# Kernel optimization log

Hardware: AMD Instinct MI355X
Metric: run time of the kernel (lower is better)

## Reference

```python
import jax, jax.numpy as jnp
import numpy as np

B, Z, H, T = 256, 512, 2048, 16
EPS = 1e-5

def _normalize(v):
    return v / (jnp.linalg.norm(v) + 1e-12)

def setup_inputs() -> dict:
    key = jax.random.key(0)
    ks = jax.random.split(key, 10)
    s = lambda fan: 1.0 / np.sqrt(fan)
    return {
        "z": jax.random.normal(ks[0], (B, Z), dtype=jnp.float32),
        "fc_w": jax.random.normal(ks[1], (Z, Z), dtype=jnp.float32) * s(Z),
        "fc_b": jnp.zeros((Z,), dtype=jnp.float32),
        "fc_u": _normalize(jax.random.normal(ks[2], (Z,), dtype=jnp.float32)),
        "w_ih": jax.random.normal(ks[3], (3 * H, Z), dtype=jnp.float32) * s(Z),
        "w_hh": jax.random.normal(ks[4], (3 * H, H), dtype=jnp.float32) * s(H),
        "b_ih": jnp.zeros((3 * H,), dtype=jnp.float32).at[H:2 * H].set(1.0),  # forget-gate bias init
        "b_hh": jnp.zeros((3 * H,), dtype=jnp.float32),
        "lin_w": jax.random.normal(ks[5], (Z, H), dtype=jnp.float32) * s(H),
        "lin_b": jnp.zeros((Z,), dtype=jnp.float32),
    }

def _spectral_norm(w, u):
    # one torch-style power iteration (u, v treated as constants)
    v = jax.lax.stop_gradient(_normalize(w.T @ u))
    u1 = jax.lax.stop_gradient(_normalize(w @ v))
    sigma = u1 @ (w @ v)
    return w / sigma

def reference(z, fc_w, fc_b, fc_u, w_ih, w_hh, b_ih, b_hh, lin_w, lin_b):
    # spectral-norm linear: h0 = z @ (W/sigma)^T + b
    w_sn = _spectral_norm(fc_w, fc_u)
    x0 = z @ w_sn.T + fc_b                      # [B, Z]
    h0 = jnp.zeros((B, H), dtype=z.dtype)       # initHidden

    def step(carry, _):
        x, h = carry
        gi = x @ w_ih.T + b_ih                  # [B, 3H]
        gh = h @ w_hh.T + b_hh                  # [B, 3H]
        i_r, i_z, i_n = jnp.split(gi, 3, axis=1)
        h_r, h_z, h_n = jnp.split(gh, 3, axis=1)
        r = jax.nn.sigmoid(i_r + h_r)
        u = jax.nn.sigmoid(i_z + h_z)
        n = jnp.tanh(i_n + r * h_n)
        h_new = (1.0 - u) * n + u * h
        x_new = h_new @ lin_w.T + lin_b         # [B, Z] fed back as next input
        return (x_new, h_new), x_new

    _, outs = jax.lax.scan(step, (x0, h0), None, length=T)  # [T, B, Z]

    # per-timestep BatchNorm1d(affine=False), training-mode batch stats
    mean = jnp.mean(outs, axis=1, keepdims=True)
    var = jnp.mean((outs - mean) ** 2, axis=1, keepdims=True)
    y = (outs - mean) / jnp.sqrt(var + EPS)     # [T, B, Z]

    y = jnp.transpose(y, (1, 0, 2))             # [B, T, Z]
    return y.reshape(-1, Z)                     # [B*T, Z]
```

## Files before the change

### kernel.cpp

```cpp
#include <hip/hip_runtime.h>
#include <hip/hip_bf16.h>
#include <cstdint>
#include <cstddef>

#define B_  256
#define Z_  512
#define H_  2048
#define T_  16
#define H3_ 6144

using short8  = __attribute__((ext_vector_type(8))) short;
using bf16x8  = __attribute__((ext_vector_type(8))) __bf16;
using f32x4   = __attribute__((ext_vector_type(4))) float;
using f32x16  = __attribute__((ext_vector_type(16))) float;

__device__ __forceinline__ f32x4 mfma_bf16(short8 a, short8 b, f32x4 c) {
  return __builtin_amdgcn_mfma_f32_16x16x32_bf16(
      __builtin_bit_cast(bf16x8, a), __builtin_bit_cast(bf16x8, b), c, 0, 0, 0);
}
__device__ __forceinline__ f32x16 mfma_bf16_32(short8 a, short8 b, f32x16 c) {
  return __builtin_amdgcn_mfma_f32_32x32x16_bf16(
      __builtin_bit_cast(bf16x8, a), __builtin_bit_cast(bf16x8, b), c, 0, 0, 0);
}

__device__ __forceinline__ unsigned short f2bf(float f) {
  unsigned int u = __builtin_bit_cast(unsigned int, f);
  u = (u + 0x7FFFu + ((u >> 16) & 1u)) >> 16;
  return (unsigned short)u;
}

__device__ __forceinline__ float sigmoidf_(float x) { return 1.0f / (1.0f + __expf(-x)); }

__device__ __forceinline__ int swz(int row, int chunk) {
  return row * 64 + ((chunk ^ (row & 7)) << 3);
}

__global__ __launch_bounds__(256, 2) void gru_step3(
    const unsigned short* __restrict__ A, int K,
    const unsigned short* __restrict__ Wr,
    const unsigned short* __restrict__ Wz,
    const unsigned short* __restrict__ Wn,
    const unsigned short* __restrict__ Whn,
    const float* __restrict__ cr, const float* __restrict__ cz,
    const float* __restrict__ cn, const float* __restrict__ chn,
    float hn_scale,
    const float* __restrict__ h_old,
    float* __restrict__ h_new,
    unsigned short* __restrict__ h_hist)
{
  __shared__ __align__(16) unsigned short sbuf[2][10240];
  __shared__ float LDSf[4][32][33];
  const int bid = blockIdx.x, tid = threadIdx.x;
  const int xcd = bid & 7, rst = bid >> 3;
  const int m_idx = rst & 7, gg = rst >> 3;
  const int grp = gg * 8 + xcd;
  const int m0 = m_idx * 32;
  const int gh0 = grp * 32;
  const int wave = tid >> 6, lane = tid & 63;
  const int lh = lane >> 5, l31 = lane & 31;

  const int arow = tid >> 3, achk = tid & 7;
  const int wrow = tid >> 1, wc0 = (tid & 1) * 4;
  const unsigned short* wsrc =
      (wrow < 32) ? Wr : (wrow < 64) ? Wz : (wrow < 96) ? Wn : Whn;
  const size_t aoff = (size_t)(m0 + arow) * K + achk * 8;
  const size_t woff = (size_t)(gh0 + (wrow & 31)) * K + wc0 * 8;
  const int sa_d = swz(arow, achk);
  const int sw_d0 = 2048 + swz(wrow, wc0 + 0);
  const int sw_d1 = 2048 + swz(wrow, wc0 + 1);
  const int sw_d2 = 2048 + swz(wrow, wc0 + 2);
  const int sw_d3 = 2048 + swz(wrow, wc0 + 3);

  uint4 Aa, Aw0, Aw1, Aw2, Aw3;
  uint4 Ba, Bw0, Bw1, Bw2, Bw3;

#define LDSET(a, w0, w1, w2, w3, k0)                      \
  {                                                        \
    const int kk_ = (k0);                                  \
    a  = *(const uint4*)(A    + aoff + kk_);               \
    w0 = *(const uint4*)(wsrc + woff + kk_);               \
    w1 = *(const uint4*)(wsrc + woff + kk_ + 8);           \
    w2 = *(const uint4*)(wsrc + woff + kk_ + 16);          \
    w3 = *(const uint4*)(wsrc + woff + kk_ + 24);          \
  }
#define STAGE(s, a, w0, w1, w2, w3)                        \
  {                                                        \
    unsigned short* b_ = sbuf[s];                          \
    *(uint4*)(b_ + sa_d)  = a;                             \
    *(uint4*)(b_ + sw_d0) = w0;                            \
    *(uint4*)(b_ + sw_d1) = w1;                            \
    *(uint4*)(b_ + sw_d2) = w2;                            \
    *(uint4*)(b_ + sw_d3) = w3;                            \
  }

  f32x16 acc = {};
#define COMP(s)                                                            \
  {                                                                        \
    const unsigned short* b_ = sbuf[s];                                    \
    _Pragma("unroll")                                                      \
    for (int ks = 0; ks < 4; ++ks) {                                       \
      short8 af = *(const short8*)(b_ + swz(l31, ks * 2 + lh));            \
      short8 wf = *(const short8*)(b_ + 2048 + swz(wave * 32 + l31, ks * 2 + lh)); \
      acc = mfma_bf16_32(af, wf, acc);                                     \
    }                                                                      \
  }

  const int nIter = K >> 6;
  LDSET(Aa, Aw0, Aw1, Aw2, Aw3, 0);
  LDSET(Ba, Bw0, Bw1, Bw2, Bw3, 64);
  for (int it = 0; it < nIter; it += 2) {
    STAGE(0, Aa, Aw0, Aw1, Aw2, Aw3);
    __syncthreads();
    { const int kn = (it + 2 < nIter) ? ((it + 2) << 6) : 0;
      LDSET(Aa, Aw0, Aw1, Aw2, Aw3, kn); }
    COMP(0);
    STAGE(1, Ba, Bw0, Bw1, Bw2, Bw3);
    __syncthreads();
    { const int kn = (it + 3 < nIter) ? ((it + 3) << 6) : 64;
      LDSET(Ba, Bw0, Bw1, Bw2, Bw3, kn); }
    COMP(1);
  }
#undef LDSET
#undef STAGE
#undef COMP

#pragma unroll
  for (int reg = 0; reg < 16; ++reg) {
    const int row = (reg & 3) + 8 * (reg >> 2) + 4 * lh;
    LDSf[wave][row][l31] = acc[reg];
  }
  __syncthreads();
  {
    const int row = tid >> 3, c0 = (tid & 7) * 4;
    const int grow = m0 + row;
#pragma unroll
    for (int j = 0; j < 4; ++j) {
      const int col = c0 + j;
      const int gcol = gh0 + col;
      const float R   = sigmoidf_(LDSf[0][row][col] + cr[gcol]);
      const float U   = sigmoidf_(LDSf[1][row][col] + cz[gcol]);
      const float HNv = hn_scale * LDSf[3][row][col] + chn[gcol];
      const float Nv  = tanhf(LDSf[2][row][col] + cn[gcol] + R * HNv);
      const float ho  = h_old ? h_old[(size_t)grow * H_ + gcol] : 0.0f;
      const float hv  = (1.0f - U) * Nv + U * ho;
      h_new[(size_t)grow * H_ + gcol]  = hv;
      h_hist[(size_t)grow * H_ + gcol] = f2bf(hv);
    }
  }
}

__global__ __launch_bounds__(256) void gemm_bt(
    const unsigned short* __restrict__ A,
    const unsigned short* __restrict__ Bw,
    int K,
    const float* __restrict__ addsrc, int add_ld,
    const float* __restrict__ bias,
    const float* __restrict__ scale_ptr,
    unsigned short* __restrict__ out_bf,
    float* __restrict__ out_f, int ldo)
{
  __shared__ unsigned short sA[32 * 64];
  __shared__ unsigned short sB[64 * 64];
  const int tid  = threadIdx.x;
  const int m0   = blockIdx.x * 32, n0 = blockIdx.y * 64;
  const int wave = tid >> 6, lane = tid & 63;
  const int wr = wave & 1, wc = wave >> 1;
  const int q = lane >> 4, c16 = lane & 15;
  const int lr = tid >> 3, lc8 = tid & 7;
  f32x4 acc0 = {}, acc1 = {};
  const size_t rowA  = (size_t)(m0 + lr) * K;
  const size_t rowB0 = (size_t)(n0 + lr) * K;
  const size_t rowB1 = (size_t)(n0 + 32 + lr) * K;
  for (int k0 = 0; k0 < K; k0 += 64) {
    const int gc = k0 + lc8 * 8;
    uint4 ra  = *(const uint4*)(A  + rowA  + gc);
    uint4 rb0 = *(const uint4*)(Bw + rowB0 + gc);
    uint4 rb1 = *(const uint4*)(Bw + rowB1 + gc);
    __syncthreads();
    *(uint4*)(sA + swz(lr, lc8))      = ra;
    *(uint4*)(sB + swz(lr, lc8))      = rb0;
    *(uint4*)(sB + swz(32 + lr, lc8)) = rb1;
    __syncthreads();
#pragma unroll
    for (int kk = 0; kk < 2; ++kk) {
      const int arow = wr * 16 + c16;
      short8 af = *(const short8*)(sA + swz(arow, kk * 4 + q));
      const int brow = wc * 32 + c16;
      short8 b0 = *(const short8*)(sB + swz(brow, kk * 4 + q));
      acc0 = mfma_bf16(af, b0, acc0);
      short8 b1 = *(const short8*)(sB + swz(brow + 16, kk * 4 + q));
      acc1 = mfma_bf16(af, b1, acc1);
    }
  }
  const float scale = scale_ptr ? *scale_ptr : 1.0f;
#pragma unroll
  for (int cf = 0; cf < 2; ++cf) {
    f32x4 a = cf ? acc1 : acc0;
#pragma unroll
    for (int v = 0; v < 4; ++v) {
      const int row = m0 + wr * 16 + q * 4 + v;
      const int col = n0 + wc * 32 + cf * 16 + c16;
      float val = a[v] * scale;
      if (addsrc) val += addsrc[(size_t)row * add_ld + col];
      if (bias)   val += bias[col];
      if (out_f)  out_f[(size_t)row * ldo + col] = val;
      if (out_bf) out_bf[(size_t)row * ldo + col] = f2bf(val);
    }
  }
}

__global__ __launch_bounds__(256) void gemm_bt64(
    const unsigned short* __restrict__ A,
    const unsigned short* __restrict__ Bw,
    int K,
    const float* __restrict__ addsrc, int add_ld,
    const float* __restrict__ bias,
    unsigned short* __restrict__ out_bf,
    float* __restrict__ out_f, int ldo)
{
  __shared__ unsigned short sA[64 * 64];
  __shared__ unsigned short sB[64 * 64];
  const int tid  = threadIdx.x;
  const int m0   = blockIdx.x * 64, n0 = blockIdx.y * 64;
  const int wave = tid >> 6, lane = tid & 63;
  const int wr = wave & 1, wc = wave >> 1;
  const int q = lane >> 4, c16 = lane & 15;
  const int lr = tid >> 3, lc8 = tid & 7;
  f32x4 acc[2][2] = {};
  const size_t aoff = (size_t)(m0 + lr) * K;
  const size_t boff = (size_t)(n0 + lr) * K;
  const size_t s32  = (size_t)32 * K;

  uint4 ra0, ra1, rb0, rb1;
  auto LOAD = [&](int k0) {
    const int gc = k0 + lc8 * 8;
    ra0 = *(const uint4*)(A  + aoff + gc);
    ra1 = *(const uint4*)(A  + aoff + s32 + gc);
    rb0 = *(const uint4*)(Bw + boff + gc);
    rb1 = *(const uint4*)(Bw + boff + s32 + gc);
  };

  const int nIter = K >> 6;
  LOAD(0);
  for (int it = 0; it < nIter; ++it) {
    __syncthreads();
    *(uint4*)(sA + swz(lr, lc8))      = ra0;
    *(uint4*)(sA + swz(lr + 32, lc8)) = ra1;
    *(uint4*)(sB + swz(lr, lc8))      = rb0;
    *(uint4*)(sB + swz(lr + 32, lc8)) = rb1;
    __syncthreads();
    if (it + 1 < nIter) LOAD((it + 1) << 6);
#pragma unroll
    for (int kk = 0; kk < 2; ++kk) {
      short8 af0 = *(const short8*)(sA + swz(wr * 32 + c16,      kk * 4 + q));
      short8 af1 = *(const short8*)(sA + swz(wr * 32 + 16 + c16, kk * 4 + q));
      short8 bf0 = *(const short8*)(sB + swz(wc * 32 + c16,      kk * 4 + q));
      short8 bf1 = *(const short8*)(sB + swz(wc * 32 + 16 + c16, kk * 4 + q));
      acc[0][0] = mfma_bf16(af0, bf0, acc[0][0]);
      acc[0][1] = mfma_bf16(af0, bf1, acc[0][1]);
      acc[1][0] = mfma_bf16(af1, bf0, acc[1][0]);
      acc[1][1] = mfma_bf16(af1, bf1, acc[1][1]);
    }
  }
#pragma unroll
  for (int i = 0; i < 2; ++i) {
#pragma unroll
    for (int j = 0; j < 2; ++j) {
#pragma unroll
      for (int v = 0; v < 4; ++v) {
        const int row = m0 + wr * 32 + i * 16 + q * 4 + v;
        const int col = n0 + wc * 32 + j * 16 + c16;
        float val = acc[i][j][v];
        if (addsrc) val += addsrc[(size_t)row * add_ld + col];
        if (bias)   val += bias[col];
        if (out_f)  out_f[(size_t)row * ldo + col] = val;
        if (out_bf) out_bf[(size_t)row * ldo + col] = f2bf(val);
      }
    }
  }
}

__global__ __launch_bounds__(256) void quant_all(
    const float* __restrict__ z, const float* __restrict__ fc_w,
    const float* __restrict__ w_ih, const float* __restrict__ w_hh,
    const float* __restrict__ lin_w,
    unsigned short* __restrict__ z_q, unsigned short* __restrict__ fc_w_q,
    unsigned short* __restrict__ w_ih_q, unsigned short* __restrict__ w_hhn_q,
    unsigned short* __restrict__ lin_w_q)
{
  const int i = blockIdx.x * 256 + threadIdx.x;
  if (i >= 2195456) return;
  const float4* src; ushort4* dst; int idx;
  if (i < 32768)        { src = (const float4*)z;     dst = (ushort4*)z_q;     idx = i; }
  else if (i < 98304)   { src = (const float4*)fc_w;  dst = (ushort4*)fc_w_q;  idx = i - 32768; }
  else if (i < 884736)  { src = (const float4*)w_ih;  dst = (ushort4*)w_ih_q;  idx = i - 98304; }
  else if (i < 1933312) { src = (const float4*)(w_hh + (size_t)2 * H_ * H_);
                          dst = (ushort4*)w_hhn_q;    idx = i - 884736; }
  else                  { src = (const float4*)lin_w; dst = (ushort4*)lin_w_q; idx = i - 1933312; }
  float4 v = src[idx];
  ushort4 o; o.x = f2bf(v.x); o.y = f2bf(v.y); o.z = f2bf(v.z); o.w = f2bf(v.w);
  dst[idx] = o;
}

__global__ __launch_bounds__(256) void transq(const float* __restrict__ s,
                                              unsigned short* __restrict__ d) {
  __shared__ float tile[32][33];
  const int tx = threadIdx.x & 31, ty = threadIdx.x >> 5;
  const int k0 = blockIdx.x * 32, z0 = blockIdx.y * 32;
#pragma unroll
  for (int j = 0; j < 4; ++j)
    tile[ty + j * 8][tx] = s[(size_t)(z0 + ty + j * 8) * H_ + k0 + tx];
  __syncthreads();
#pragma unroll
  for (int j = 0; j < 4; ++j)
    d[(size_t)(k0 + ty + j * 8) * Z_ + z0 + tx] = f2bf(tile[tx][ty + j * 8]);
}

__global__ void sigma1(const float* __restrict__ W, const float* __restrict__ u,
                       float* __restrict__ t1) {
  __shared__ float part[4][64];
  const int lane = threadIdx.x & 63, wv = threadIdx.x >> 6;
  const int col = blockIdx.x * 64 + lane;
  float s = 0.f;
  for (int r = wv * 128; r < wv * 128 + 128; ++r)
    s += W[(size_t)r * Z_ + col] * u[r];
  part[wv][lane] = s;
  __syncthreads();
  if (wv == 0)
    t1[col] = part[0][lane] + part[1][lane] + part[2][lane] + part[3][lane];
}

__global__ void sigma1b(const float* __restrict__ t1, float* __restrict__ invn) {
  __shared__ float red[256];
  int t = threadIdx.x;
  float v0 = t1[t], v1 = t1[t + 256];
  red[t] = v0 * v0 + v1 * v1;
  __syncthreads();
  for (int s = 128; s > 0; s >>= 1) {
    if (t < s) red[t] += red[t + s];
    __syncthreads();
  }
  if (t == 0) invn[0] = 1.0f / (sqrtf(red[0]) + 1e-12f);
}

__global__ void sigma2(const float* __restrict__ W, const float* __restrict__ t1,
                       const float* __restrict__ invn, float* __restrict__ t2) {
  const int lane = threadIdx.x & 63, wv = threadIdx.x >> 6;
  const int row = blockIdx.x * 4 + wv;
  float s = 0.f;
  for (int c = lane; c < Z_; c += 64) s += W[(size_t)row * Z_ + c] * t1[c];
#pragma unroll
  for (int off = 32; off > 0; off >>= 1) s += __shfl_down(s, off);
  if (lane == 0) t2[row] = s * invn[0];
}

__global__ void sigma3(const float* __restrict__ t2, float* __restrict__ inv_sig) {
  __shared__ float red[256];
  int t = threadIdx.x;
  float v0 = t2[t], v1 = t2[t + 256];
  red[t] = v0 * v0 + v1 * v1;
  __syncthreads();
  for (int s = 128; s > 0; s >>= 1) {
    if (t < s) red[t] += red[t + s];
    __syncthreads();
  }
  if (t == 0) {
    float s2  = red[0];
    float sig = s2 / (sqrtf(s2) + 1e-12f);
    inv_sig[0] = 1.0f / sig;
  }
}

__global__ __launch_bounds__(256) void dots_k(const float* __restrict__ w,
                                              const float* __restrict__ lb,
                                              float* __restrict__ dvec) {
  const int wave = threadIdx.x >> 6, lane = threadIdx.x & 63;
#pragma unroll
  for (int i = 0; i < 4; ++i) {
    int row = blockIdx.x * 16 + wave * 4 + i;
    float s = 0.f;
    for (int c = lane; c < Z_; c += 64) s += w[(size_t)row * Z_ + c] * lb[c];
#pragma unroll
    for (int off = 32; off > 0; off >>= 1) s += __shfl_down(s, off);
    if (lane == 0) dvec[row] = s;
  }
}

__global__ void consts_k(const float* __restrict__ b_ih, const float* __restrict__ b_hh,
                         const float* __restrict__ dvec,
                         float* __restrict__ c0r, float* __restrict__ c0z,
                         float* __restrict__ c0n,
                         float* __restrict__ c1r, float* __restrict__ c1z,
                         float* __restrict__ c1n, float* __restrict__ chn) {
  int j = blockIdx.x * 256 + threadIdx.x;
  float br = b_ih[j], bz = b_ih[H_ + j], bn = b_ih[2 * H_ + j];
  float hr = b_hh[j], hz = b_hh[H_ + j], hn = b_hh[2 * H_ + j];
  c0r[j] = br + hr; c0z[j] = bz + hz; c0n[j] = bn; chn[j] = hn;
  c1r[j] = br + hr + dvec[j];
  c1z[j] = bz + hz + dvec[H_ + j];
  c1n[j] = bn + dvec[2 * H_ + j];
}

__global__ __launch_bounds__(256) void bn_k(const float* __restrict__ outs,
                                            float* __restrict__ y) {
  __shared__ float s_sum[4][64], s_sq[4][64], s_mean[64], s_inv[64];
  const int t = blockIdx.x, zb = blockIdx.y;
  const int zl = threadIdx.x & 63, bp = threadIdx.x >> 6;
  const int z = zb * 64 + zl;
  float sum = 0.f, sq = 0.f;
  for (int b = bp * 64; b < bp * 64 + 64; ++b) {
    float v = outs[(size_t)(t * 256 + b) * Z_ + z];
    sum += v; sq += v * v;
  }
  s_sum[bp][zl] = sum; s_sq[bp][zl] = sq;
  __syncthreads();
  if (bp == 0) {
    float S = s_sum[0][zl] + s_sum[1][zl] + s_sum[2][zl] + s_sum[3][zl];
    float Q = s_sq[0][zl] + s_sq[1][zl] + s_sq[2][zl] + s_sq[3][zl];
    float mean = S * (1.0f / 256.0f);
    float var  = Q * (1.0f / 256.0f) - mean * mean;
    s_mean[zl] = mean;
    s_inv[zl]  = rsqrtf(var + 1e-5f);
  }
  __syncthreads();
  const float mean = s_mean[zl], inv = s_inv[zl];
  for (int b = bp * 64; b < bp * 64 + 64; ++b) {
    float v = outs[(size_t)(t * 256 + b) * Z_ + z];
    y[(size_t)(b * T_ + t) * Z_ + z] = (v - mean) * inv;
  }
}

extern "C" void kernel_launch(void* const* d_in, const int* in_sizes, int n_in,
                              void* d_out, int out_size, void* d_ws, size_t ws_size,
                              hipStream_t stream) {
  const float* z     = (const float*)d_in[0];
  const float* fc_w  = (const float*)d_in[1];
  const float* fc_b  = (const float*)d_in[2];
  const float* fc_u  = (const float*)d_in[3];
  const float* w_ih  = (const float*)d_in[4];
  const float* w_hh  = (const float*)d_in[5];
  const float* b_ih  = (const float*)d_in[6];
  const float* b_hh  = (const float*)d_in[7];
  const float* lin_w = (const float*)d_in[8];
  const float* lin_b = (const float*)d_in[9];
  float* out = (float*)d_out;

  char* ws = (char*)d_ws;
  size_t off = 0;
  auto alloc = [&](size_t bytes) -> void* {
    off = (off + 255) & ~(size_t)255;
    void* p = ws + off;
    off += bytes;
    return p;
  };
  unsigned short* w_ih_q   = (unsigned short*)alloc((size_t)H3_ * Z_ * 2);
  unsigned short* w_hhn_q  = (unsigned short*)alloc((size_t)H_ * H_ * 2);
  unsigned short* lin_w_q  = (unsigned short*)alloc((size_t)Z_ * H_ * 2);
  unsigned short* lin_wT_q = (unsigned short*)alloc((size_t)Z_ * H_ * 2);
  unsigned short* fc_w_q   = (unsigned short*)alloc((size_t)Z_ * Z_ * 2);
  unsigned short* z_q      = (unsigned short*)alloc((size_t)B_ * Z_ * 2);
  unsigned short* x0_q     = (unsigned short*)alloc((size_t)B_ * Z_ * 2);
  unsigned short* Wsum_r   = (unsigned short*)alloc((size_t)H_ * H_ * 2);
  unsigned short* Wsum_z   = (unsigned short*)alloc((size_t)H_ * H_ * 2);
  unsigned short* Wn_c     = (unsigned short*)alloc((size_t)H_ * H_ * 2);
  unsigned short* Hhist    = (unsigned short*)alloc((size_t)T_ * B_ * H_ * 2);
  float* h_f32 = (float*)alloc((size_t)2 * B_ * H_ * 4);
  float* outs  = (float*)alloc((size_t)T_ * B_ * Z_ * 4);
  float* c0r = (float*)alloc(H_ * 4);
  float* c0z = (float*)alloc(H_ * 4);
  float* c0n = (float*)alloc(H_ * 4);
  float* c1r = (float*)alloc(H_ * 4);
  float* c1z = (float*)alloc(H_ * 4);
  float* c1n = (float*)alloc(H_ * 4);
  float* chn = (float*)alloc(H_ * 4);
  float* dvec = (float*)alloc(H3_ * 4);
  float* t1v = (float*)alloc(Z_ * 4);
  float* t2v = (float*)alloc(Z_ * 4);
  float* invn = (float*)alloc(256);
  float* invsig = (float*)alloc(256);
  (void)in_sizes; (void)n_in; (void)out_size; (void)ws_size;

  quant_all<<<dim3((2195456 + 255) / 256), 256, 0, stream>>>(
      z, fc_w, w_ih, w_hh, lin_w, z_q, fc_w_q, w_ih_q, w_hhn_q, lin_w_q);
  transq<<<dim3(64, 16), 256, 0, stream>>>(lin_w, lin_wT_q);
  sigma1<<<8, 256, 0, stream>>>(fc_w, fc_u, t1v);
  sigma1b<<<1, 256, 0, stream>>>(t1v, invn);
  sigma2<<<128, 256, 0, stream>>>(fc_w, t1v, invn, t2v);
  sigma3<<<1, 256, 0, stream>>>(t2v, invsig);
  dots_k<<<384, 256, 0, stream>>>(w_ih, lin_b, dvec);
  consts_k<<<8, 256, 0, stream>>>(b_ih, b_hh, dvec, c0r, c0z, c0n, c1r, c1z, c1n, chn);

  gemm_bt<<<dim3(B_ / 32, Z_ / 64), 256, 0, stream>>>(
      z_q, fc_w_q, Z_, nullptr, 0, fc_b, invsig, x0_q, nullptr, Z_);

  for (int g = 0; g < 3; ++g) {
    const float* adds = (g < 2) ? (w_hh + (size_t)g * H_ * H_) : nullptr;
    unsigned short* outw = (g == 0) ? Wsum_r : (g == 1) ? Wsum_z : Wn_c;
    gemm_bt64<<<dim3(H_ / 64, H_ / 64), 256, 0, stream>>>(
        w_ih_q + (size_t)g * H_ * Z_, lin_wT_q, Z_, adds, H_, nullptr,
        outw, nullptr, H_);
  }

  for (int t = 0; t < T_; ++t) {
    if (t == 0) {
      gru_step3<<<512, 256, 0, stream>>>(
          x0_q, Z_,
          w_ih_q, w_ih_q + (size_t)H_ * Z_, w_ih_q + (size_t)2 * H_ * Z_,
          w_ih_q ,
          c0r, c0z, c0n, chn, 0.0f, nullptr, h_f32, Hhist);
    } else {
      gru_step3<<<512, 256, 0, stream>>>(
          Hhist + (size_t)(t - 1) * B_ * H_, H_,
          Wsum_r, Wsum_z, Wn_c, w_hhn_q,
          c1r, c1z, c1n, chn, 1.0f,
          h_f32 + (size_t)((t - 1) & 1) * B_ * H_,
          h_f32 + (size_t)(t & 1) * B_ * H_,
          Hhist + (size_t)t * B_ * H_);
    }
  }

  gemm_bt64<<<dim3(T_ * B_ / 64, Z_ / 64), 256, 0, stream>>>(
      Hhist, lin_w_q, H_, nullptr, 0, lin_b, nullptr, outs, Z_);

  bn_k<<<dim3(T_, Z_ / 64), 256, 0, stream>>>(outs, out);
}
```

Before: 483.0 us.

## Enlarge GRU step tile to 64 rows with 512-thread blocks

The recurrent GRU step kernel now processes 64 batch rows per block instead of 32, using 8 waves (4 gates × 2 row halves) and 256 blocks instead of 512. Each weight tile loaded into shared memory is reused across twice as many batch rows, halving total weight traffic from global memory per step. The cost is fewer blocks than CUs, which lowers occupancy, and more shared memory per block.

```diff
diff --git a/kernel.cpp b/kernel.cpp
--- a/kernel.cpp
+++ b/kernel.cpp
@@ -35,7 +35,7 @@
   return row * 64 + ((chunk ^ (row & 7)) << 3);
 }
 
-__global__ __launch_bounds__(256, 2) void gru_step3(
+__global__ __launch_bounds__(512, 1) void gru_step4(
     const unsigned short* __restrict__ A, int K,
     const unsigned short* __restrict__ Wr,
     const unsigned short* __restrict__ Wz,
@@ -48,49 +48,44 @@
     float* __restrict__ h_new,
     unsigned short* __restrict__ h_hist)
 {
-  __shared__ __align__(16) unsigned short sbuf[2][10240];
-  __shared__ float LDSf[4][32][33];
+  __shared__ __align__(16) unsigned short sbuf[2][12288];
+  __shared__ float LDSf[4][64][33];
   const int bid = blockIdx.x, tid = threadIdx.x;
   const int xcd = bid & 7, rst = bid >> 3;
-  const int m_idx = rst & 7, gg = rst >> 3;
+  const int m_idx = rst & 3, gg = rst >> 2;
   const int grp = gg * 8 + xcd;
-  const int m0 = m_idx * 32;
+  const int m0 = m_idx * 64;
   const int gh0 = grp * 32;
   const int wave = tid >> 6, lane = tid & 63;
+  const int gate = wave & 3, mh = wave >> 2;
   const int lh = lane >> 5, l31 = lane & 31;
 
   const int arow = tid >> 3, achk = tid & 7;
-  const int wrow = tid >> 1, wc0 = (tid & 1) * 4;
+  const int wrow = tid >> 2, wc0 = (tid & 3) * 2;
   const unsigned short* wsrc =
       (wrow < 32) ? Wr : (wrow < 64) ? Wz : (wrow < 96) ? Wn : Whn;
   const size_t aoff = (size_t)(m0 + arow) * K + achk * 8;
   const size_t woff = (size_t)(gh0 + (wrow & 31)) * K + wc0 * 8;
-  const int sa_d = swz(arow, achk);
-  const int sw_d0 = 2048 + swz(wrow, wc0 + 0);
-  const int sw_d1 = 2048 + swz(wrow, wc0 + 1);
-  const int sw_d2 = 2048 + swz(wrow, wc0 + 2);
-  const int sw_d3 = 2048 + swz(wrow, wc0 + 3);
-
-  uint4 Aa, Aw0, Aw1, Aw2, Aw3;
-  uint4 Ba, Bw0, Bw1, Bw2, Bw3;
-
-#define LDSET(a, w0, w1, w2, w3, k0)                      \
+  const int sa_d  = swz(arow, achk);
+  const int sw_d0 = 4096 + swz(wrow, wc0 + 0);
+  const int sw_d1 = 4096 + swz(wrow, wc0 + 1);
+
+  uint4 Aa, Aw0, Aw1;
+  uint4 Ba, Bw0, Bw1;
+
+#define LDSET(a, w0, w1, k0)                               \
   {                                                        \
     const int kk_ = (k0);                                  \
     a  = *(const uint4*)(A    + aoff + kk_);               \
     w0 = *(const uint4*)(wsrc + woff + kk_);               \
     w1 = *(const uint4*)(wsrc + woff + kk_ + 8);           \
-    w2 = *(const uint4*)(wsrc + woff + kk_ + 16);          \
-    w3 = *(const uint4*)(wsrc + woff + kk_ + 24);          \
-  }
-#define STAGE(s, a, w0, w1, w2, w3)                        \
+  }
+#define STAGE(s, a, w0, w1)                                \
   {                                                        \
     unsigned short* b_ = sbuf[s];                          \
     *(uint4*)(b_ + sa_d)  = a;                             \
     *(uint4*)(b_ + sw_d0) = w0;                            \
     *(uint4*)(b_ + sw_d1) = w1;                            \
-    *(uint4*)(b_ + sw_d2) = w2;                            \
-    *(uint4*)(b_ + sw_d3) = w3;                            \
   }
 
   f32x16 acc = {};
@@ -99,25 +94,25 @@
     const unsigned short* b_ = sbuf[s];                                    \
     _Pragma("unroll")                                                      \
     for (int ks = 0; ks < 4; ++ks) {                                       \
-      short8 af = *(const short8*)(b_ + swz(l31, ks * 2 + lh));            \
-      short8 wf = *(const short8*)(b_ + 2048 + swz(wave * 32 + l31, ks * 2 + lh)); \
+      short8 af = *(const short8*)(b_ + swz(mh * 32 + l31, ks * 2 + lh));  \
+      short8 wf = *(const short8*)(b_ + 4096 + swz(gate * 32 + l31, ks * 2 + lh)); \
       acc = mfma_bf16_32(af, wf, acc);                                     \
     }                                                                      \
   }
 
   const int nIter = K >> 6;
-  LDSET(Aa, Aw0, Aw1, Aw2, Aw3, 0);
-  LDSET(Ba, Bw0, Bw1, Bw2, Bw3, 64);
+  LDSET(Aa, Aw0, Aw1, 0);
+  LDSET(Ba, Bw0, Bw1, 64);
   for (int it = 0; it < nIter; it += 2) {
-    STAGE(0, Aa, Aw0, Aw1, Aw2, Aw3);
+    STAGE(0, Aa, Aw0, Aw1);
     __syncthreads();
     { const int kn = (it + 2 < nIter) ? ((it + 2) << 6) : 0;
-      LDSET(Aa, Aw0, Aw1, Aw2, Aw3, kn); }
+      LDSET(Aa, Aw0, Aw1, kn); }
     COMP(0);
-    STAGE(1, Ba, Bw0, Bw1, Bw2, Bw3);
+    STAGE(1, Ba, Bw0, Bw1);
     __syncthreads();
     { const int kn = (it + 3 < nIter) ? ((it + 3) << 6) : 64;
-      LDSET(Ba, Bw0, Bw1, Bw2, Bw3, kn); }
+      LDSET(Ba, Bw0, Bw1, kn); }
     COMP(1);
   }
 #undef LDSET
@@ -126,8 +121,8 @@
 
 #pragma unroll
   for (int reg = 0; reg < 16; ++reg) {
-    const int row = (reg & 3) + 8 * (reg >> 2) + 4 * lh;
-    LDSf[wave][row][l31] = acc[reg];
+    const int trow = (reg & 3) + 8 * (reg >> 2) + 4 * lh;
+    LDSf[gate][mh * 32 + trow][l31] = acc[reg];
   }
   __syncthreads();
   {
@@ -503,13 +498,13 @@
 
   for (int t = 0; t < T_; ++t) {
     if (t == 0) {
-      gru_step3<<<512, 256, 0, stream>>>(
+      gru_step4<<<256, 512, 0, stream>>>(
           x0_q, Z_,
           w_ih_q, w_ih_q + (size_t)H_ * Z_, w_ih_q + (size_t)2 * H_ * Z_,
           w_ih_q ,
           c0r, c0z, c0n, chn, 0.0f, nullptr, h_f32, Hhist);
     } else {
-      gru_step3<<<512, 256, 0, stream>>>(
+      gru_step4<<<256, 512, 0, stream>>>(
           Hhist + (size_t)(t - 1) * B_ * H_, H_,
           Wsum_r, Wsum_z, Wn_c, w_hhn_q,
           c1r, c1z, c1n, chn, 1.0f,
```

After: 402.9 us, median of 2. 1.2x faster.
